# Performance work log

Measured on AMD Instinct MI355X. Metric: run time of the kernel, lower is better.

The kernel has to match this reference:

```python
import jax, jax.numpy as jnp
import numpy as np

N = 100_000   # nodes
E = 1_600_000 # edges (avg degree 16)
D = 32        # input = hidden = output channels (module defaults)
L = 3         # num_layers


def setup_inputs() -> dict:
    key = jax.random.key(0)
    ks = jax.random.split(key, 6)
    X = jax.random.normal(ks[0], (N, D), jnp.float32)
    edge_index = jax.random.randint(ks[1], (2, E), 0, N)
    edge_weight = jax.random.uniform(ks[2], (E,), jnp.float32)
    # 8 GCNConv layers per GConvLSTM: x_i, h_i, x_f, h_f, x_c, h_c, x_o, h_o
    conv_w = jax.random.normal(ks[3], (L, 8, D, D), jnp.float32) * np.float32(1.0 / np.sqrt(D))
    conv_b = jnp.zeros((L, 8, D), jnp.float32)
    # peephole weights w_c_i, w_c_f, w_c_o (glorot) and biases b_i, b_f, b_c, b_o (zeros)
    wc = jax.random.normal(ks[4], (L, 3, D), jnp.float32) * np.float32(0.1)
    bg = jnp.zeros((L, 4, D), jnp.float32)
    return dict(X=X, edge_index=edge_index, edge_weight=edge_weight,
                conv_w=conv_w, conv_b=conv_b, wc=wc, bg=bg)


def _gcn_norm(edge_index, edge_weight, n):
    # PyG gcn_norm (sym): add self loops with weight 1, then D^-1/2 A D^-1/2
    loop = jnp.arange(n)
    src = jnp.concatenate([edge_index[0], loop])
    dst = jnp.concatenate([edge_index[1], loop])
    w = jnp.concatenate([edge_weight, jnp.ones((n,), edge_weight.dtype)])
    deg = jax.ops.segment_sum(w, dst, num_segments=n)
    dinv = jnp.where(deg > 0, jax.lax.rsqrt(deg), jnp.zeros_like(deg))
    return src, dst, dinv[src] * w * dinv[dst]


def reference(X, edge_index, edge_weight, conv_w, conv_b, wc, bg):
    n = X.shape[0]
    src, dst, nw = _gcn_norm(edge_index, edge_weight, n)

    def gcn(x, W, b):
        xw = x @ W                                   # [N, D] linear transform
        agg = jax.ops.segment_sum(nw[:, None] * xw[src], dst, num_segments=n)
        return agg + b

    out = X
    for l in range(conv_w.shape[0]):
        x = out
        H = jnp.zeros((n, conv_w.shape[-1]), x.dtype)  # hidden state init (None -> zeros)
        C = jnp.zeros_like(H)                          # cell state init
        Wl, bl = conv_w[l], conv_b[l]
        I = jax.nn.sigmoid(gcn(x, Wl[0], bl[0]) + gcn(H, Wl[1], bl[1]) + wc[l, 0] * C + bg[l, 0])
        F = jax.nn.sigmoid(gcn(x, Wl[2], bl[2]) + gcn(H, Wl[3], bl[3]) + wc[l, 1] * C + bg[l, 1])
        T = jnp.tanh(gcn(x, Wl[4], bl[4]) + gcn(H, Wl[5], bl[5]) + bg[l, 2])
        C = F * C + I * T
        O = jax.nn.sigmoid(gcn(x, Wl[6], bl[6]) + gcn(H, Wl[7], bl[7]) + wc[l, 2] * C + bg[l, 3])
        out = O * jnp.tanh(C)
    return out
```

## Files before the change

kernel.cpp:

```cpp
#include <hip/hip_runtime.h>
#include <math.h>

#define TPB 256
#define NBMAX 2048

__device__ __forceinline__ float fsig(float x) {
    return __builtin_amdgcn_rcpf(1.f + __expf(-x));
}
__device__ __forceinline__ float ftanh(float x) {
    float t = __expf(2.f * fabsf(x));
    float r = 1.f - 2.f * __builtin_amdgcn_rcpf(t + 1.f);
    return copysignf(r, x);
}

__global__ __launch_bounds__(256) void k_zero(int* __restrict__ p, int n) {
    int i = blockIdx.x * 256 + threadIdx.x;
    if (i < n) p[i] = 0;
}


__global__ __launch_bounds__(256) void k_bhist(const int* __restrict__ ei,
                                               int* __restrict__ bhist, int E, int NB) {
    __shared__ int h[NBMAX];
    for (int i = threadIdx.x; i < NB; i += 256) h[i] = 0;
    __syncthreads();
    int stride = gridDim.x * 256;
    for (int e = blockIdx.x * 256 + threadIdx.x; e < E; e += stride)
        atomicAdd(&h[ei[E + e] >> 8], 1);
    __syncthreads();
    for (int i = threadIdx.x; i < NB; i += 256) if (h[i]) atomicAdd(&bhist[i], h[i]);
}

__global__ __launch_bounds__(256) void k_bscan(const int* __restrict__ bhist,
                                               int* __restrict__ bbase, int* __restrict__ bfill,
                                               int* __restrict__ row_start,
                                               int NB, int N, int E) {
    __shared__ int tsum[256];
    int tid = threadIdx.x;
    int per = (NB + 255) / 256;
    int loc[8]; int tot = 0;
    int base = tid * per;
#pragma unroll
    for (int j = 0; j < 8; j++) {
        int i = base + j;
        int v = (j < per && i < NB) ? bhist[i] : 0;
        loc[j] = v; tot += v;
    }
    tsum[tid] = tot;
    __syncthreads();
    for (int off = 1; off < 256; off <<= 1) {
        int t = (tid >= off) ? tsum[tid - off] : 0;
        __syncthreads();
        tsum[tid] += t;
        __syncthreads();
    }
    int run = tsum[tid] - tot;
#pragma unroll
    for (int j = 0; j < 8; j++) {
        int i = base + j;
        if (j < per && i < NB) { bbase[i] = run; bfill[i] = run; run += loc[j]; }
    }
    if (tid == 0) { bbase[NB] = E; row_start[N] = E; }
}

__global__ __launch_bounds__(256) void k_bin(const int* __restrict__ ei,
                                             const float* __restrict__ ew,
                                             int* bfill, int2* __restrict__ ebuf,
                                             int E, int NB) {
    __shared__ int h[NBMAX];
    __shared__ int gb[NBMAX];
    const int EPT = 16;
    int tid = threadIdx.x;
    int base = blockIdx.x * 256 * EPT;
    for (int i = tid; i < NB; i += 256) h[i] = 0;
    __syncthreads();
    int src[EPT]; float w[EPT]; int bkt[EPT]; int lrank[EPT];
#pragma unroll
    for (int j = 0; j < EPT; j++) {
        int e = base + j * 256 + tid;
        if (e < E) {
            src[j] = ei[e]; int d = ei[E + e]; w[j] = ew[e];
            int b = d >> 8;
            bkt[j] = b | ((d & 255) << 16);
            lrank[j] = atomicAdd(&h[b], 1);
        } else bkt[j] = -1;
    }
    __syncthreads();
    for (int i = tid; i < NB; i += 256) gb[i] = h[i] ? atomicAdd(&bfill[i], h[i]) : 0;
    __syncthreads();
#pragma unroll
    for (int j = 0; j < EPT; j++) {
        if (bkt[j] >= 0) {
            int b = bkt[j] & 0xFFFF, dlow = (bkt[j] >> 16) & 0xFF;
            int2 v; v.x = src[j] | (dlow << 24); v.y = __float_as_int(w[j]);
            ebuf[gb[b] + lrank[j]] = v;
        }
    }
}

__global__ __launch_bounds__(256) void k_bucket(const int2* __restrict__ ebuf,
                                                const int* __restrict__ bbase,
                                                int2* __restrict__ csr,
                                                int2* __restrict__ esl,
                                                int* __restrict__ row_start,
                                                float* __restrict__ dinv,
                                                const float4* __restrict__ X4,
                                                float4* __restrict__ Y4,
                                                int N, int E) {
    __shared__ int lcnt[256];
    __shared__ float wsum[256];
    __shared__ int lstart[256];
    __shared__ int sc[256];
    __shared__ float sdinv[256];
    int b = blockIdx.x, tid = threadIdx.x;
    int beg = bbase[b], end = bbase[b + 1];
    lcnt[tid] = 0; wsum[tid] = 0.f;
    __syncthreads();
    for (int i = beg + tid; i < end; i += 256) {
        int2 v = ebuf[i];
        int dlow = ((unsigned)v.x) >> 24;
        atomicAdd(&lcnt[dlow], 1);
        atomicAdd(&wsum[dlow], __int_as_float(v.y));
    }
    __syncthreads();
    int myc = lcnt[tid];
    sc[tid] = myc;
    __syncthreads();
    for (int off = 1; off < 256; off <<= 1) {
        int t = (tid >= off) ? sc[tid - off] : 0;
        __syncthreads();
        sc[tid] += t;
        __syncthreads();
    }
    lstart[tid] = sc[tid] - myc;
    int node = (b << 8) + tid;
    float dv = rsqrtf(1.0f + wsum[tid]);
    sdinv[tid] = dv;
    if (node < N) {
        row_start[node] = beg + sc[tid] - myc;
        dinv[node] = dv;
    }
    lcnt[tid] = 0;
    __syncthreads();
    size_t nodeBase = (size_t)(b << 8) * 32;
    for (int i = beg + tid; i < end; i += 256) {
        int2 v = ebuf[i];
        int dlow = ((unsigned)v.x) >> 24;
        int rank = atomicAdd(&lcnt[dlow], 1);
        int2 o; o.x = v.x & 0x00FFFFFF; o.y = v.y;
        csr[beg + lstart[dlow] + rank] = o;
        if (rank < 32) esl[nodeBase + dlow * 32 + rank] = o;
    }
    __syncthreads();
    int nNodes = N - (b << 8); if (nNodes > 256) nNodes = 256;
    for (int i = tid; i < nNodes * 32; i += 256) {
        int r = i >> 5, j = i & 31;
        if (j >= lcnt[r]) { int2 z; z.x = 0; z.y = 0; esl[nodeBase + i] = z; }
    }
    int limit = nNodes * 8;
    size_t base4 = ((size_t)b << 8) * 8;
    for (int i = tid; i < limit; i += 256) {
        float4 v = X4[base4 + i];
        float d = sdinv[i >> 3];
        float4 o; o.x = v.x * d; o.y = v.y * d; o.z = v.z * d; o.w = v.w * d;
        Y4[base4 + i] = o;
    }
}


__global__ __launch_bounds__(256) void k_gather(const float4* __restrict__ Y4,
                                                const int2* __restrict__ esl,
                                                const int* __restrict__ row_start,
                                                const int2* __restrict__ csr,
                                                const float* __restrict__ dinv,
                                                float4* __restrict__ AX4, int N) {
    int wid = (blockIdx.x * blockDim.x + threadIdx.x) >> 6;
    if (wid >= N) return;
    int lane = threadIdx.x & 63;
    int q = lane >> 3, c4 = lane & 7;
    const int2* ep = esl + (size_t)wid * 32 + q;
    int2 p0 = ep[0], p1 = ep[8], p2 = ep[16], p3 = ep[24];
    float di = dinv[wid];
    float4 self = Y4[(size_t)wid * 8 + c4];
    int rs = row_start[wid], re = row_start[wid + 1];
    float4 y0 = Y4[(size_t)p0.x * 8 + c4];
    float4 y1 = Y4[(size_t)p1.x * 8 + c4];
    float4 y2 = Y4[(size_t)p2.x * 8 + c4];
    float4 y3 = Y4[(size_t)p3.x * 8 + c4];
    float w0 = __int_as_float(p0.y), w1 = __int_as_float(p1.y);
    float w2 = __int_as_float(p2.y), w3 = __int_as_float(p3.y);
    float4 acc1, acc2;
    if (q == 0) acc1 = self; else { acc1.x = acc1.y = acc1.z = acc1.w = 0.f; }
    acc2.x = acc2.y = acc2.z = acc2.w = 0.f;
    acc1.x += w0 * y0.x; acc1.y += w0 * y0.y; acc1.z += w0 * y0.z; acc1.w += w0 * y0.w;
    acc2.x += w1 * y1.x; acc2.y += w1 * y1.y; acc2.z += w1 * y1.z; acc2.w += w1 * y1.w;
    acc1.x += w2 * y2.x; acc1.y += w2 * y2.y; acc1.z += w2 * y2.z; acc1.w += w2 * y2.w;
    acc2.x += w3 * y3.x; acc2.y += w3 * y3.y; acc2.z += w3 * y3.z; acc2.w += w3 * y3.w;
    if (re - rs > 32) {
        for (int e = rs + 32 + q; e < re; e += 8) {
            int2 t = csr[e];
            float4 yt = Y4[(size_t)t.x * 8 + c4];
            float wt = __int_as_float(t.y);
            acc1.x += wt * yt.x; acc1.y += wt * yt.y; acc1.z += wt * yt.z; acc1.w += wt * yt.w;
        }
    }
    acc1.x += acc2.x; acc1.y += acc2.y; acc1.z += acc2.z; acc1.w += acc2.w;
#pragma unroll
    for (int off = 8; off <= 32; off <<= 1) {
        acc1.x += __shfl_xor(acc1.x, off);
        acc1.y += __shfl_xor(acc1.y, off);
        acc1.z += __shfl_xor(acc1.z, off);
        acc1.w += __shfl_xor(acc1.w, off);
    }
    if (lane < 8) {
        float4 o; o.x = acc1.x * di; o.y = acc1.y * di; o.z = acc1.z * di; o.w = acc1.w * di;
        AX4[(size_t)wid * 8 + c4] = o;
    }
}

__global__ __launch_bounds__(256) void k_gates(const float* __restrict__ AX,
                                               const float* __restrict__ cw,
                                               const float* __restrict__ cb,
                                               const float* __restrict__ wc,
                                               const float* __restrict__ bg,
                                               const float* __restrict__ dinv,
                                               float* __restrict__ outRaw,
                                               float* __restrict__ outY,
                                               int N, int l, int isLast) {
    __shared__ float Ws[32][96];
    __shared__ float Xs[128][33];
    __shared__ float bS[96];
    __shared__ float wcs[32];
    __shared__ float sdv[128];
    int tid = threadIdx.x;
    for (int i = tid; i < 3072; i += 256) {
        int k = i / 96, ccol = i - k * 96;
        int g = ccol >> 5, o = ccol & 31;
        int j = (g == 0) ? 0 : ((g == 1) ? 4 : 6);
        Ws[k][ccol] = cw[(((l * 8 + j) * 32) + k) * 32 + o];
    }
    if (tid < 32) {
        int c = tid;
        bS[c]      = cb[((l * 8 + 0) * 32) + c] + cb[((l * 8 + 1) * 32) + c] + bg[((l * 4 + 0) * 32) + c];
        bS[32 + c] = cb[((l * 8 + 4) * 32) + c] + cb[((l * 8 + 5) * 32) + c] + bg[((l * 4 + 2) * 32) + c];
        bS[64 + c] = cb[((l * 8 + 6) * 32) + c] + cb[((l * 8 + 7) * 32) + c] + bg[((l * 4 + 3) * 32) + c];
        wcs[c]     = wc[((l * 3 + 2) * 32) + c];
    }
    int row0 = blockIdx.x * 128;
    for (int i = tid; i < 4096; i += 256) {
        int r = i >> 5, k = i & 31; int gr = row0 + r;
        Xs[r][k] = (gr < N) ? AX[(size_t)gr * 32 + k] : 0.f;
    }
    if (tid < 128) {
        int gr = row0 + tid;
        sdv[tid] = (gr < N) ? dinv[gr] : 0.f;
    }
    __syncthreads();
    int r0 = tid >> 3, g8 = tid & 7, cbase = g8 * 4;
    float aI[4][4], aT[4][4], aO[4][4];
#pragma unroll
    for (int j = 0; j < 4; j++)
#pragma unroll
        for (int cc = 0; cc < 4; cc++) { aI[j][cc] = 0.f; aT[j][cc] = 0.f; aO[j][cc] = 0.f; }
#pragma unroll 4
    for (int k = 0; k < 32; k++) {
        float4 wI = *(const float4*)&Ws[k][cbase];
        float4 wT = *(const float4*)&Ws[k][32 + cbase];
        float4 wO = *(const float4*)&Ws[k][64 + cbase];
#pragma unroll
        for (int j = 0; j < 4; j++) {
            float xv = Xs[r0 + 32 * j][k];
            aI[j][0] += xv * wI.x; aI[j][1] += xv * wI.y; aI[j][2] += xv * wI.z; aI[j][3] += xv * wI.w;
            aT[j][0] += xv * wT.x; aT[j][1] += xv * wT.y; aT[j][2] += xv * wT.z; aT[j][3] += xv * wT.w;
            aO[j][0] += xv * wO.x; aO[j][1] += xv * wO.y; aO[j][2] += xv * wO.z; aO[j][3] += xv * wO.w;
        }
    }
#pragma unroll
    for (int j = 0; j < 4; j++) {
        int r = r0 + 32 * j;
        int gn = row0 + r;
        if (gn >= N) continue;
        float di = sdv[r];
        float4 v;
        float res[4];
#pragma unroll
        for (int cc = 0; cc < 4; cc++) {
            int c = cbase + cc;
            float I = fsig(aI[j][cc] + bS[c]);
            float T = ftanh(aT[j][cc] + bS[32 + c]);
            float C = I * T;
            float O = fsig(aO[j][cc] + wcs[c] * C + bS[64 + c]);
            float val = O * ftanh(C);
            res[cc] = isLast ? val : di * val;
        }
        v.x = res[0]; v.y = res[1]; v.z = res[2]; v.w = res[3];
        float* dst = isLast ? outRaw : outY;
        *(float4*)&dst[(size_t)gn * 32 + cbase] = v;
    }
}

extern "C" void kernel_launch(void* const* d_in, const int* in_sizes, int n_in,
                              void* d_out, int out_size, void* d_ws, size_t ws_size,
                              hipStream_t stream) {
    const float* X  = (const float*)d_in[0];
    const int*   ei = (const int*)d_in[1];
    const float* ew = (const float*)d_in[2];
    const float* cw = (const float*)d_in[3];
    const float* cb = (const float*)d_in[4];
    const float* wc = (const float*)d_in[5];
    const float* bg = (const float*)d_in[6];
    int N = in_sizes[0] / 32;
    int E = in_sizes[2];
    int L = in_sizes[3] / (8 * 32 * 32);
    float* out = (float*)d_out;
    int NB = (N + 255) >> 8;

    char* p = (char*)d_ws;
    auto alloc = [&](size_t bytes) -> char* {
        char* r = p; p += (bytes + 255) & ~(size_t)255; return r;
    };
    int*   bhist     = (int*)alloc((size_t)NB * 4);
    int*   bbase     = (int*)alloc((size_t)(NB + 1) * 4);
    int*   bfill     = (int*)alloc((size_t)NB * 4);
    int*   row_start = (int*)alloc((size_t)(N + 1) * 4);
    float* dinv      = (float*)alloc((size_t)N * 4);
    int2*  ebuf      = (int2*)alloc((size_t)E * 8);
    int2*  csr       = (int2*)alloc((size_t)E * 8);
    int2*  esl       = (int2*)alloc((size_t)N * 32 * 8);
    float* Y         = (float*)alloc((size_t)N * 32 * 4);
    float* AX        = (float*)alloc((size_t)N * 32 * 4);

    k_zero<<<(NB + 255) / 256, 256, 0, stream>>>(bhist, NB);
    k_bhist<<<512, 256, 0, stream>>>(ei, bhist, E, NB);
    k_bscan<<<1, 256, 0, stream>>>(bhist, bbase, bfill, row_start, NB, N, E);
    int nBin = (E + 4095) / 4096;
    k_bin<<<nBin, 256, 0, stream>>>(ei, ew, bfill, ebuf, E, NB);
    k_bucket<<<NB, 256, 0, stream>>>(ebuf, bbase, csr, esl, row_start, dinv,
                                     (const float4*)X, (float4*)Y, N, E);

    for (int l = 0; l < L; l++) {
        k_gather<<<(N + 3) / 4, 256, 0, stream>>>((const float4*)Y, esl, row_start,
                                                  csr, dinv, (float4*)AX, N);
        k_gates<<<(N + 127) / 128, 256, 0, stream>>>(AX, cw, cb, wc, bg, dinv,
                                                     out, Y, N, l, l == L - 1);
    }
}
```

Measured before the change: 259.8 us.

## Replace full CSR with ELL slots plus atomic overflow list for high-degree tails

Drops the full CSR build (count pass, scan, CSR scatter) in the bucket kernel and folds the weighted-degree sum into the single slot-assignment pass. Edges beyond the 32 fixed slots per node go to an overflow list, and a new small tail kernel adds them into AX with atomics after each gather. This removes one pass over edges and the CSR write, and takes the variable-length loop out of the gather. In exchange it adds a kernel launch per layer, a global atomic counter, and a fixed 65536-entry overflow buffer that could overflow on skewed inputs. Float atomics also make the summation order nondeterministic.

```diff
diff --git a/kernel.cpp b/kernel.cpp
--- a/kernel.cpp
+++ b/kernel.cpp
@@ -33,8 +33,7 @@
 
 __global__ __launch_bounds__(256) void k_bscan(const int* __restrict__ bhist,
                                                int* __restrict__ bbase, int* __restrict__ bfill,
-                                               int* __restrict__ row_start,
-                                               int NB, int N, int E) {
+                                               int NB, int E) {
     __shared__ int tsum[256];
     int tid = threadIdx.x;
     int per = (NB + 255) / 256;
@@ -60,7 +59,7 @@
         int i = base + j;
         if (j < per && i < NB) { bbase[i] = run; bfill[i] = run; run += loc[j]; }
     }
-    if (tid == 0) { bbase[NB] = E; row_start[N] = E; }
+    if (tid == 0) bbase[NB] = E;
 }
 
 __global__ __launch_bounds__(256) void k_bin(const int* __restrict__ ei,
@@ -100,58 +99,40 @@
 
 __global__ __launch_bounds__(256) void k_bucket(const int2* __restrict__ ebuf,
                                                 const int* __restrict__ bbase,
-                                                int2* __restrict__ csr,
                                                 int2* __restrict__ esl,
-                                                int* __restrict__ row_start,
+                                                int4* __restrict__ ovbuf,
+                                                int* __restrict__ ovcnt,
                                                 float* __restrict__ dinv,
                                                 const float4* __restrict__ X4,
                                                 float4* __restrict__ Y4,
                                                 int N, int E) {
     __shared__ int lcnt[256];
     __shared__ float wsum[256];
-    __shared__ int lstart[256];
-    __shared__ int sc[256];
     __shared__ float sdinv[256];
     int b = blockIdx.x, tid = threadIdx.x;
     int beg = bbase[b], end = bbase[b + 1];
     lcnt[tid] = 0; wsum[tid] = 0.f;
     __syncthreads();
-    for (int i = beg + tid; i < end; i += 256) {
-        int2 v = ebuf[i];
-        int dlow = ((unsigned)v.x) >> 24;
-        atomicAdd(&lcnt[dlow], 1);
-        atomicAdd(&wsum[dlow], __int_as_float(v.y));
-    }
-    __syncthreads();
-    int myc = lcnt[tid];
-    sc[tid] = myc;
-    __syncthreads();
-    for (int off = 1; off < 256; off <<= 1) {
-        int t = (tid >= off) ? sc[tid - off] : 0;
-        __syncthreads();
-        sc[tid] += t;
-        __syncthreads();
-    }
-    lstart[tid] = sc[tid] - myc;
-    int node = (b << 8) + tid;
-    float dv = rsqrtf(1.0f + wsum[tid]);
-    sdinv[tid] = dv;
-    if (node < N) {
-        row_start[node] = beg + sc[tid] - myc;
-        dinv[node] = dv;
-    }
-    lcnt[tid] = 0;
-    __syncthreads();
     size_t nodeBase = (size_t)(b << 8) * 32;
     for (int i = beg + tid; i < end; i += 256) {
         int2 v = ebuf[i];
         int dlow = ((unsigned)v.x) >> 24;
+        unsafeAtomicAdd(&wsum[dlow], __int_as_float(v.y));
         int rank = atomicAdd(&lcnt[dlow], 1);
         int2 o; o.x = v.x & 0x00FFFFFF; o.y = v.y;
-        csr[beg + lstart[dlow] + rank] = o;
-        if (rank < 32) esl[nodeBase + dlow * 32 + rank] = o;
-    }
-    __syncthreads();
+        if (rank < 32) {
+            esl[nodeBase + dlow * 32 + rank] = o;
+        } else {
+            int oi = atomicAdd(ovcnt, 1);
+            int4 q; q.x = o.x; q.y = (b << 8) + dlow; q.z = o.y; q.w = 0;
+            ovbuf[oi] = q;
+        }
+    }
+    __syncthreads();
+    float dv = rsqrtf(1.0f + wsum[tid]);
+    sdinv[tid] = dv;
+    int node = (b << 8) + tid;
+    if (node < N) dinv[node] = dv;
     int nNodes = N - (b << 8); if (nNodes > 256) nNodes = 256;
     for (int i = tid; i < nNodes * 32; i += 256) {
         int r = i >> 5, j = i & 31;
@@ -170,8 +151,6 @@
 
 __global__ __launch_bounds__(256) void k_gather(const float4* __restrict__ Y4,
                                                 const int2* __restrict__ esl,
-                                                const int* __restrict__ row_start,
-                                                const int2* __restrict__ csr,
                                                 const float* __restrict__ dinv,
                                                 float4* __restrict__ AX4, int N) {
     int wid = (blockIdx.x * blockDim.x + threadIdx.x) >> 6;
@@ -182,7 +161,6 @@
     int2 p0 = ep[0], p1 = ep[8], p2 = ep[16], p3 = ep[24];
     float di = dinv[wid];
     float4 self = Y4[(size_t)wid * 8 + c4];
-    int rs = row_start[wid], re = row_start[wid + 1];
     float4 y0 = Y4[(size_t)p0.x * 8 + c4];
     float4 y1 = Y4[(size_t)p1.x * 8 + c4];
     float4 y2 = Y4[(size_t)p2.x * 8 + c4];
@@ -196,14 +174,6 @@
     acc2.x += w1 * y1.x; acc2.y += w1 * y1.y; acc2.z += w1 * y1.z; acc2.w += w1 * y1.w;
     acc1.x += w2 * y2.x; acc1.y += w2 * y2.y; acc1.z += w2 * y2.z; acc1.w += w2 * y2.w;
     acc2.x += w3 * y3.x; acc2.y += w3 * y3.y; acc2.z += w3 * y3.z; acc2.w += w3 * y3.w;
-    if (re - rs > 32) {
-        for (int e = rs + 32 + q; e < re; e += 8) {
-            int2 t = csr[e];
-            float4 yt = Y4[(size_t)t.x * 8 + c4];
-            float wt = __int_as_float(t.y);
-            acc1.x += wt * yt.x; acc1.y += wt * yt.y; acc1.z += wt * yt.z; acc1.w += wt * yt.w;
-        }
-    }
     acc1.x += acc2.x; acc1.y += acc2.y; acc1.z += acc2.z; acc1.w += acc2.w;
 #pragma unroll
     for (int off = 8; off <= 32; off <<= 1) {
@@ -215,6 +185,23 @@
     if (lane < 8) {
         float4 o; o.x = acc1.x * di; o.y = acc1.y * di; o.z = acc1.z * di; o.w = acc1.w * di;
         AX4[(size_t)wid * 8 + c4] = o;
+    }
+}
+
+__global__ __launch_bounds__(256) void k_tail(const float* __restrict__ Y,
+                                              const int4* __restrict__ ovbuf,
+                                              const int* __restrict__ ovcnt,
+                                              const float* __restrict__ dinv,
+                                              float* __restrict__ AX) {
+    int cnt = *ovcnt;
+    int total = cnt * 32;
+    int stride = gridDim.x * 256;
+    for (int i = blockIdx.x * 256 + threadIdx.x; i < total; i += stride) {
+        int e = i >> 5, c = i & 31;
+        int4 q = ovbuf[e];
+        int src = q.x, dst = q.y;
+        float w = __int_as_float(q.z);
+        atomicAdd(&AX[(size_t)dst * 32 + c], dinv[dst] * w * Y[(size_t)src * 32 + c]);
     }
 }
 
@@ -319,28 +306,29 @@
     auto alloc = [&](size_t bytes) -> char* {
         char* r = p; p += (bytes + 255) & ~(size_t)255; return r;
     };
-    int*   bhist     = (int*)alloc((size_t)NB * 4);
+    int*   bhist     = (int*)alloc((size_t)(NB + 1) * 4);
     int*   bbase     = (int*)alloc((size_t)(NB + 1) * 4);
     int*   bfill     = (int*)alloc((size_t)NB * 4);
-    int*   row_start = (int*)alloc((size_t)(N + 1) * 4);
     float* dinv      = (float*)alloc((size_t)N * 4);
     int2*  ebuf      = (int2*)alloc((size_t)E * 8);
-    int2*  csr       = (int2*)alloc((size_t)E * 8);
     int2*  esl       = (int2*)alloc((size_t)N * 32 * 8);
+    int4*  ovbuf     = (int4*)alloc((size_t)65536 * 16);
     float* Y         = (float*)alloc((size_t)N * 32 * 4);
     float* AX        = (float*)alloc((size_t)N * 32 * 4);
-
-    k_zero<<<(NB + 255) / 256, 256, 0, stream>>>(bhist, NB);
+    int*   ovcnt     = bhist + NB;
+
+    k_zero<<<(NB + 256) / 256, 256, 0, stream>>>(bhist, NB + 1);
     k_bhist<<<512, 256, 0, stream>>>(ei, bhist, E, NB);
-    k_bscan<<<1, 256, 0, stream>>>(bhist, bbase, bfill, row_start, NB, N, E);
+    k_bscan<<<1, 256, 0, stream>>>(bhist, bbase, bfill, NB, E);
     int nBin = (E + 4095) / 4096;
     k_bin<<<nBin, 256, 0, stream>>>(ei, ew, bfill, ebuf, E, NB);
-    k_bucket<<<NB, 256, 0, stream>>>(ebuf, bbase, csr, esl, row_start, dinv,
+    k_bucket<<<NB, 256, 0, stream>>>(ebuf, bbase, esl, ovbuf, ovcnt, dinv,
                                      (const float4*)X, (float4*)Y, N, E);
 
     for (int l = 0; l < L; l++) {
-        k_gather<<<(N + 3) / 4, 256, 0, stream>>>((const float4*)Y, esl, row_start,
-                                                  csr, dinv, (float4*)AX, N);
+        k_gather<<<(N + 3) / 4, 256, 0, stream>>>((const float4*)Y, esl, dinv,
+                                                  (float4*)AX, N);
+        k_tail<<<16, 256, 0, stream>>>(Y, ovbuf, ovcnt, dinv, AX);
         k_gates<<<(N + 127) / 128, 256, 0, stream>>>(AX, cw, cb, wc, bg, dinv,
                                                      out, Y, N, l, l == L - 1);
     }
```

New measurement: 248.0 us. 4.5% less time.
